# Kernel optimization log

Measured on AMD Instinct MI355X. Metric: run time of the kernel, lower is better.

Reference implementation:

```python
import jax, jax.numpy as jnp
import numpy as np

B, F, NQ, DT, TS, K = 16384, 256, 2048, 256, 16, 8
GH, SH, CALH = 128, 128, 16
SPD = DT + TS
SPH = max(int(SPD * 0.25), 16)
CD = DT + 3 + TS + 3  # h_base + y_base + 3 gate stats + z_top + |d_safe| + |d_spec| = 278
CH = max(int(CD * 0.25), 16)
RES_SCALE = 0.1


def _ln(x, g, b):
    m = x.mean(-1, keepdims=True)
    v = ((x - m) ** 2).mean(-1, keepdims=True)
    return (x - m) * jax.lax.rsqrt(v + 1e-5) * g + b


def _resmlp(x, lg, lb, w1, b1, w2, b2):
    h = jnp.maximum(_ln(x, lg, lb) @ w1 + b1, 0.0)
    return h @ w2 + b2


def setup_inputs() -> dict:
    key = jax.random.key(0)
    ks = iter(jax.random.split(key, 48))
    def nrm(shape, s=0.05):
        return jax.random.normal(next(ks), shape, jnp.float32) * s
    d = {}
    d["x_num"] = jax.random.normal(next(ks), (B, F), jnp.float32)
    d["robust_center"] = nrm((1, F), 0.1)
    d["robust_scale"] = jax.random.uniform(next(ks), (1, F), jnp.float32, 0.5, 1.5)
    d["quantile_sorted"] = jnp.sort(jax.random.normal(next(ks), (NQ, F), jnp.float32), axis=0)
    d["stem_w1"] = nrm((3, CALH)); d["stem_b1"] = jnp.zeros((CALH,))
    d["stem_w2"] = nrm((CALH, CALH)); d["stem_b2"] = jnp.zeros((CALH,))
    d["stem_w3"] = nrm((CALH, 1)); d["stem_b3"] = jnp.zeros((1,))
    d["gate_w1"] = nrm((F, GH)); d["gate_b1"] = jnp.zeros((GH,))
    d["gate_w2"] = nrm((GH, F)); d["gate_b2"] = jnp.zeros((F,))
    d["bb_w"] = nrm((F, DT)); d["bb_b"] = jnp.zeros((DT,))
    d["base_w"] = nrm((DT, 1)); d["base_b"] = jnp.zeros((1,))
    d["safe_lg"] = jnp.ones((DT,)); d["safe_lb"] = jnp.zeros((DT,))
    d["safe_w1"] = nrm((DT, SH)); d["safe_b1"] = jnp.zeros((SH,))
    d["safe_w2"] = nrm((SH, 1)); d["safe_b2"] = jnp.zeros((1,))
    d["top_w1"] = nrm((1, TS)); d["top_b1"] = jnp.zeros((TS,))
    d["top_w2"] = nrm((TS, TS)); d["top_b2"] = jnp.zeros((TS,))
    d["spec_lg"] = jnp.ones((SPD,)); d["spec_lb"] = jnp.zeros((SPD,))
    d["spec_w1"] = nrm((SPD, SPH)); d["spec_b1"] = jnp.zeros((SPH,))
    d["spec_w2"] = nrm((SPH, 1)); d["spec_b2"] = jnp.zeros((1,))
    d["conf_lg"] = jnp.ones((CD,)); d["conf_lb"] = jnp.zeros((CD,))
    d["conf_w1"] = nrm((CD, CH)); d["conf_b1"] = jnp.zeros((CH,))
    d["conf_w2"] = nrm((CH, 1)); d["conf_b2"] = jnp.full((1,), -2.0)  # gamma_init_bias
    return d


def _forward(x_num, robust_center, robust_scale, quantile_sorted,
             stem_w1, stem_b1, stem_w2, stem_b2, stem_w3, stem_b3,
             gate_w1, gate_b1, gate_w2, gate_b2,
             bb_w, bb_b, base_w, base_b,
             safe_lg, safe_lb, safe_w1, safe_b1, safe_w2, safe_b2,
             top_w1, top_b1, top_w2, top_b2,
             spec_lg, spec_lb, spec_w1, spec_b1, spec_w2, spec_b2,
             conf_lg, conf_lb, conf_w1, conf_b1, conf_w2, conf_b2):
    # --- calibration views ---
    x_robust = (x_num - robust_center) / robust_scale
    ranks = jax.vmap(jnp.searchsorted, in_axes=(1, 1), out_axes=1)(
        jax.lax.stop_gradient(quantile_sorted), jax.lax.stop_gradient(x_num))  # [B,F] int
    x_quant = jnp.clip(ranks.astype(jnp.float32) / (NQ - 1.0), 0.0, 1.0)
    x_views = jnp.stack([x_num, x_robust, x_quant], axis=-1)  # [B,F,3]
    h = jnp.maximum(x_views @ stem_w1 + stem_b1, 0.0)
    h = jnp.maximum(h @ stem_w2 + stem_b2, 0.0)
    resid = jnp.tanh((h @ stem_w3 + stem_b3)[..., 0])
    x_cal = x_num + RES_SCALE * resid
    # --- input gate ---
    g = jax.nn.sigmoid(jnp.maximum(x_cal @ gate_w1 + gate_b1, 0.0) @ gate_w2 + gate_b2)
    x_gated = x_cal * g
    # --- backbone (stand-in for TMLPBackbone.encode_hidden) ---
    h_base = jnp.maximum(x_gated @ bb_w + bb_b, 0.0)  # [B,DT]
    y_base = h_base @ base_w + base_b  # [B,1]
    gate_mean = g.mean(axis=1, keepdims=True)
    gate_max = g.max(axis=1, keepdims=True)
    gate_std = g.std(axis=1, keepdims=True)  # ddof=0, matches unbiased=False
    delta_safe = _resmlp(h_base, safe_lg, safe_lb, safe_w1, safe_b1, safe_w2, safe_b2)
    # --- top-k feature gather ---
    topk_g, topk_idx = jax.lax.top_k(g, K)
    topk_x = jnp.take_along_axis(x_cal, topk_idx, axis=1)
    topk_w = topk_g / (topk_g.sum(axis=1, keepdims=True) + 1e-6)
    xw = (topk_x * topk_w)[..., None]  # [B,K,1]
    tok = jnp.maximum(xw @ top_w1 + top_b1, 0.0) @ top_w2 + top_b2  # [B,K,TS]
    z_top = tok.mean(axis=1)  # [B,TS]
    delta_spec = _resmlp(jnp.concatenate([h_base, z_top], axis=1),
                         spec_lg, spec_lb, spec_w1, spec_b1, spec_w2, spec_b2)
    conf_in = jnp.concatenate([h_base, y_base, gate_mean, gate_max, gate_std,
                               z_top, jnp.abs(delta_safe), jnp.abs(delta_spec)], axis=1)
    gamma = jax.nn.sigmoid(_resmlp(conf_in, conf_lg, conf_lb, conf_w1, conf_b1, conf_w2, conf_b2))
    return (y_base + delta_safe + gamma * delta_spec)[:, 0]


def reference(x_num, robust_center, robust_scale, quantile_sorted,
              stem_w1, stem_b1, stem_w2, stem_b2, stem_w3, stem_b3,
              gate_w1, gate_b1, gate_w2, gate_b2,
              bb_w, bb_b, base_w, base_b,
              safe_lg, safe_lb, safe_w1, safe_b1, safe_w2, safe_b2,
              top_w1, top_b1, top_w2, top_b2,
              spec_lg, spec_lb, spec_w1, spec_b1, spec_w2, spec_b2,
              conf_lg, conf_lb, conf_w1, conf_b1, conf_w2, conf_b2):
    return _forward(x_num, robust_center, robust_scale, quantile_sorted,
                    stem_w1, stem_b1, stem_w2, stem_b2, stem_w3, stem_b3,
                    gate_w1, gate_b1, gate_w2, gate_b2,
                    bb_w, bb_b, base_w, base_b,
                    safe_lg, safe_lb, safe_w1, safe_b1, safe_w2, safe_b2,
                    top_w1, top_b1, top_w2, top_b2,
                    spec_lg, spec_lb, spec_w1, spec_b1, spec_w2, spec_b2,
                    conf_lg, conf_lb, conf_w1, conf_b1, conf_w2, conf_b2)
```

## Files before the change

kernel.cpp:

```cpp
#include <hip/hip_runtime.h>
#include <math.h>

static constexpr int B  = 16384;
static constexpr int F  = 256;
static constexpr int NQ = 2048;
static constexpr int TS = 16;
static constexpr int KTOP = 8;
static constexpr int SPD = 272;
static constexpr int SPH = 68;
static constexpr int CD  = 278;
static constexpr int CH  = 69;

typedef __attribute__((ext_vector_type(8))) short bf16x8;
typedef __attribute__((ext_vector_type(4))) float f32x4;

__device__ inline short f2bf(float f) {
    unsigned u = __builtin_bit_cast(unsigned, f);
    unsigned r = (u + 0x7FFF + ((u >> 16) & 1)) >> 16;
    return (short)r;
}

__device__ inline float fast_tanh(float o) {
    o = fminf(fmaxf(o, -15.0f), 15.0f);
    float e = __expf(2.0f * o);
    return (e - 1.0f) / (e + 1.0f);
}

__device__ inline void prep_one(const float* W, short* T, int local,
                                int K, int N, int KP) {
    const int n = local / KP, k = local - n * KP;
    T[local] = (k < K && n < N) ? f2bf(W[k * N + n]) : (short)0;
}

__global__ __launch_bounds__(256) void k_prepall(
    const float* __restrict__ gate_w1, const float* __restrict__ gate_w2,
    const float* __restrict__ bb_w,    const float* __restrict__ safe_w1,
    const float* __restrict__ spec_w1, const float* __restrict__ conf_w1,
    const float* __restrict__ qs,
    short* __restrict__ w1t, short* __restrict__ w2t, short* __restrict__ bbt,
    short* __restrict__ sw1t, short* __restrict__ spw1t, short* __restrict__ cfw1t,
    float* __restrict__ qs_t)
{
    const int idx = blockIdx.x * 256 + threadIdx.x;
    if (idx < 32768)       prep_one(gate_w1, w1t,  idx,           256, 128, 256);
    else if (idx < 65536)  prep_one(gate_w2, w2t,  idx - 32768,   128, 256, 128);
    else if (idx < 131072) prep_one(bb_w,    bbt,  idx - 65536,   256, 256, 256);
    else if (idx < 163840) prep_one(safe_w1, sw1t, idx - 131072,  256, 128, 256);
    else if (idx < 200704) prep_one(spec_w1, spw1t, idx - 163840, 272, 68, 288);
    else if (idx < 237568) prep_one(conf_w1, cfw1t, idx - 200704, 278, 69, 288);
    else if (idx < 761856) {
        const int local = idx - 237568;
        const int f = local >> 11, q = local & 2047;
        qs_t[local] = qs[q * 256 + f];
    }
}

__global__ __launch_bounds__(256) void k_calib5(
    const float* __restrict__ x_num, const float* __restrict__ center,
    const float* __restrict__ scale, const float* __restrict__ qs,
    const float* __restrict__ qs_t,
    const float* __restrict__ sw1, const float* __restrict__ sb1,
    const float* __restrict__ sw2, const float* __restrict__ sb2,
    const float* __restrict__ sw3, const float* __restrict__ sb3,
    float* __restrict__ x_cal)
{
    __shared__ float cq[63 * 256];
    const int tid = threadIdx.x;
    const int f = tid;
#pragma unroll 1
    for (int j = 0; j < 63; ++j)
        cq[j * 256 + tid] = qs[(32 * (j + 1)) * 256 + tid];
    __syncthreads();

    const float c = center[f];
    const float inv_sc = 1.0f / scale[f];
    const float* colp = qs_t + (long)f * NQ;
    const long row_base = (long)blockIdx.x * 32;

#pragma unroll 1
    for (int grp = 0; grp < 4; ++grp) {
        const long r0 = row_base + grp * 8;
        float x[8], xr[8];
#pragma unroll
        for (int i = 0; i < 8; ++i) {
            x[i] = x_num[(r0 + i) * F + f];
            xr[i] = (x[i] - c) * inv_sc;
        }
        int lo[8], hi[8];
#pragma unroll
        for (int i = 0; i < 8; ++i) { lo[i] = 0; hi[i] = 63; }
#pragma unroll
        for (int it = 0; it < 6; ++it) {
            float qv[8]; int mid[8];
#pragma unroll
            for (int i = 0; i < 8; ++i) {
                mid[i] = (lo[i] + hi[i]) >> 1;
                qv[i] = cq[mid[i] * 256 + f];
            }
#pragma unroll
            for (int i = 0; i < 8; ++i) {
                if (qv[i] < x[i]) lo[i] = mid[i] + 1; else hi[i] = mid[i];
            }
        }
        int base[8];
        {
            float pm[8];
#pragma unroll
            for (int i = 0; i < 8; ++i) pm[i] = colp[lo[i] * 32 + 16];
#pragma unroll
            for (int i = 0; i < 8; ++i)
                base[i] = lo[i] * 32 + ((pm[i] < x[i]) ? 16 : 0);
        }
        float xq[8];
#pragma unroll
        for (int i = 0; i < 8; ++i) {
            const float4* wp = reinterpret_cast<const float4*>(&colp[base[i]]);
            const float4 a = wp[0], b = wp[1], d = wp[2], e = wp[3];
            int cN = 0;
            cN += (a.x < x[i]); cN += (a.y < x[i]); cN += (a.z < x[i]); cN += (a.w < x[i]);
            cN += (b.x < x[i]); cN += (b.y < x[i]); cN += (b.z < x[i]); cN += (b.w < x[i]);
            cN += (d.x < x[i]); cN += (d.y < x[i]); cN += (d.z < x[i]); cN += (d.w < x[i]);
            cN += (e.x < x[i]); cN += (e.y < x[i]); cN += (e.z < x[i]); cN += (e.w < x[i]);
            const int rank = base[i] + cN;
            xq[i] = fminf((float)rank * (1.0f / (float)(NQ - 1)), 1.0f);
        }
#pragma unroll
        for (int hgrp = 0; hgrp < 2; ++hgrp) {
            const int o4 = hgrp * 4;
            float h2[4][16];
#pragma unroll
            for (int j = 0; j < 16; ++j) {
                const float bb = sb2[j];
#pragma unroll
                for (int i = 0; i < 4; ++i) h2[i][j] = bb;
            }
#pragma unroll 4
            for (int i16 = 0; i16 < 16; ++i16) {
                const float w0 = sw1[i16], w1v = sw1[16 + i16], w2v = sw1[32 + i16];
                const float bb = sb1[i16];
                float h1v[4];
#pragma unroll
                for (int i = 0; i < 4; ++i)
                    h1v[i] = fmaxf(bb + x[o4 + i] * w0 + xr[o4 + i] * w1v + xq[o4 + i] * w2v, 0.0f);
                float wv[16];
                const float4* wr = reinterpret_cast<const float4*>(&sw2[i16 * 16]);
                *reinterpret_cast<float4*>(&wv[0])  = wr[0];
                *reinterpret_cast<float4*>(&wv[4])  = wr[1];
                *reinterpret_cast<float4*>(&wv[8])  = wr[2];
                *reinterpret_cast<float4*>(&wv[12]) = wr[3];
#pragma unroll
                for (int j = 0; j < 16; ++j) {
#pragma unroll
                    for (int i = 0; i < 4; ++i) h2[i][j] += h1v[i] * wv[j];
                }
            }
            const float b3 = sb3[0];
            float o[4] = {b3, b3, b3, b3};
#pragma unroll
            for (int j = 0; j < 16; ++j) {
                const float w3v = sw3[j];
#pragma unroll
                for (int i = 0; i < 4; ++i) o[i] += fmaxf(h2[i][j], 0.0f) * w3v;
            }
#pragma unroll
            for (int i = 0; i < 4; ++i)
                x_cal[(r0 + o4 + i) * F + f] = x[o4 + i] + 0.1f * fast_tanh(o[i]);
        }
    }
}

static constexpr int ST1 = 136;
static constexpr int ST2 = 264;

__global__ __launch_bounds__(256) void k_fused(
    const float* __restrict__ x_cal,
    const short* __restrict__ w1t, const float* __restrict__ gate_b1,
    const short* __restrict__ w2t, const float* __restrict__ gate_b2,
    const short* __restrict__ bbt, const float* __restrict__ bb_b,
    float* __restrict__ g, float* __restrict__ h_b)
{
    __shared__ short s_c1[32 * ST1];
    __shared__ short s_xg[32 * ST2];

    const int tid = threadIdx.x;
    const int wave = tid >> 6, lane = tid & 63;
    const int sub = lane & 15, quad = lane >> 4;
    const int wm = wave & 1, wn = wave >> 1;
    const long row0 = (long)blockIdx.x * 32;
    const long mrow = row0 + wm * 16 + sub;

    {
        f32x4 acc[4];
#pragma unroll
        for (int t = 0; t < 4; ++t) acc[t] = (f32x4){0, 0, 0, 0};
#pragma unroll
        for (int k0 = 0; k0 < 256; k0 += 32) {
            const float* ap = x_cal + mrow * 256 + k0 + quad * 8;
            float av[8];
            *reinterpret_cast<float4*>(&av[0]) = *reinterpret_cast<const float4*>(ap);
            *reinterpret_cast<float4*>(&av[4]) = *reinterpret_cast<const float4*>(ap + 4);
            bf16x8 af;
#pragma unroll
            for (int j = 0; j < 8; ++j) af[j] = f2bf(av[j]);
#pragma unroll
            for (int t = 0; t < 4; ++t) {
                const int col = wn * 64 + t * 16 + sub;
                const bf16x8 bf = *reinterpret_cast<const bf16x8*>(
                    &w1t[(long)col * 256 + k0 + quad * 8]);
                acc[t] = __builtin_amdgcn_mfma_f32_16x16x32_bf16(af, bf, acc[t], 0, 0, 0);
            }
        }
#pragma unroll
        for (int t = 0; t < 4; ++t) {
            const int col = wn * 64 + t * 16 + sub;
            const float bb = gate_b1[col];
#pragma unroll
            for (int r = 0; r < 4; ++r) {
                const int rowl = wm * 16 + quad * 4 + r;
                s_c1[rowl * ST1 + col] = f2bf(fmaxf(acc[t][r] + bb, 0.0f));
            }
        }
    }
    __syncthreads();

    {
        f32x4 acc[8];
#pragma unroll
        for (int t = 0; t < 8; ++t) acc[t] = (f32x4){0, 0, 0, 0};
#pragma unroll
        for (int k0 = 0; k0 < 128; k0 += 32) {
            const bf16x8 af = *reinterpret_cast<const bf16x8*>(
                &s_c1[(wm * 16 + sub) * ST1 + k0 + quad * 8]);
#pragma unroll
            for (int t = 0; t < 8; ++t) {
                const int col = wn * 128 + t * 16 + sub;
                const bf16x8 bf = *reinterpret_cast<const bf16x8*>(
                    &w2t[(long)col * 128 + k0 + quad * 8]);
                acc[t] = __builtin_amdgcn_mfma_f32_16x16x32_bf16(af, bf, acc[t], 0, 0, 0);
            }
        }
#pragma unroll
        for (int t = 0; t < 8; ++t) {
            const int col = wn * 128 + t * 16 + sub;
            const float bb = gate_b2[col];
#pragma unroll
            for (int r = 0; r < 4; ++r) {
                const int rowl = wm * 16 + quad * 4 + r;
                const float gv = 1.0f / (1.0f + __expf(-(acc[t][r] + bb)));
                g[(row0 + rowl) * 256 + col] = gv;
                const float xg = x_cal[(row0 + rowl) * 256 + col] * gv;
                s_xg[rowl * ST2 + col] = f2bf(xg);
            }
        }
    }
    __syncthreads();

    {
        f32x4 acc[8];
#pragma unroll
        for (int t = 0; t < 8; ++t) acc[t] = (f32x4){0, 0, 0, 0};
#pragma unroll
        for (int k0 = 0; k0 < 256; k0 += 32) {
            const bf16x8 af = *reinterpret_cast<const bf16x8*>(
                &s_xg[(wm * 16 + sub) * ST2 + k0 + quad * 8]);
#pragma unroll
            for (int t = 0; t < 8; ++t) {
                const int col = wn * 128 + t * 16 + sub;
                const bf16x8 bf = *reinterpret_cast<const bf16x8*>(
                    &bbt[(long)col * 256 + k0 + quad * 8]);
                acc[t] = __builtin_amdgcn_mfma_f32_16x16x32_bf16(af, bf, acc[t], 0, 0, 0);
            }
        }
#pragma unroll
        for (int t = 0; t < 8; ++t) {
            const int col = wn * 128 + t * 16 + sub;
            const float bb = bb_b[col];
#pragma unroll
            for (int r = 0; r < 4; ++r) {
                const int rowl = wm * 16 + quad * 4 + r;
                h_b[(row0 + rowl) * 256 + col] = fmaxf(acc[t][r] + bb, 0.0f);
            }
        }
    }
}

__global__ __launch_bounds__(64) void k_topk(
    const float* __restrict__ g, const float* __restrict__ x_cal,
    const float* __restrict__ tw1, const float* __restrict__ tb1,
    const float* __restrict__ tw2, const float* __restrict__ tb2,
    float* __restrict__ z_top, float* __restrict__ stats)
{
    __shared__ float s_hm[16];
    const int b = blockIdx.x;
    const int lane = threadIdx.x;
    const long base = (long)b * F;

    float gv[4];
#pragma unroll
    for (int i = 0; i < 4; ++i) gv[i] = g[base + lane + 64 * i];

    float s = gv[0] + gv[1] + gv[2] + gv[3];
    float mx = fmaxf(fmaxf(gv[0], gv[1]), fmaxf(gv[2], gv[3]));
    for (int m = 32; m; m >>= 1) {
        s  += __shfl_xor(s, m);
        mx  = fmaxf(mx, __shfl_xor(mx, m));
    }
    const float mean = s * (1.0f / 256.0f);
    float vs = 0.0f;
#pragma unroll
    for (int i = 0; i < 4; ++i) { float d = gv[i] - mean; vs += d * d; }
    for (int m = 32; m; m >>= 1) vs += __shfl_xor(vs, m);
    const float stdv = sqrtf(vs * (1.0f / 256.0f));

    float cur[4]; int curi[4];
#pragma unroll
    for (int i = 0; i < 4; ++i) { cur[i] = gv[i]; curi[i] = lane + 64 * i; }
    float tv[KTOP]; int ti[KTOP]; float vsum = 0.0f;
    for (int r = 0; r < KTOP; ++r) {
        float bv = cur[0]; int bi = curi[0];
#pragma unroll
        for (int i = 1; i < 4; ++i)
            if (cur[i] > bv || (cur[i] == bv && curi[i] < bi)) { bv = cur[i]; bi = curi[i]; }
        for (int m = 32; m; m >>= 1) {
            float ov = __shfl_xor(bv, m);
            int   oi = __shfl_xor(bi, m);
            if (ov > bv || (ov == bv && oi < bi)) { bv = ov; bi = oi; }
        }
        tv[r] = bv; ti[r] = bi; vsum += bv;
#pragma unroll
        for (int i = 0; i < 4; ++i) if (curi[i] == bi) cur[i] = -INFINITY;
    }
    const float denom = 1.0f / (vsum + 1e-6f);

    if (lane < 16) {
        float hm = 0.0f;
        for (int k = 0; k < KTOP; ++k) {
            const float xk = x_cal[base + ti[k]];
            const float xw = xk * (tv[k] * denom);
            hm += fmaxf(xw * tw1[lane] + tb1[lane], 0.0f);
        }
        s_hm[lane] = hm * (1.0f / (float)KTOP);
    }
    __syncthreads();
    if (lane < 16) {
        float z = tb2[lane];
#pragma unroll
        for (int j = 0; j < 16; ++j) z += s_hm[j] * tw2[j * 16 + lane];
        z_top[(long)b * TS + lane] = z;
    }
    if (lane == 0) {
        stats[(long)b * 4 + 0] = mean;
        stats[(long)b * 4 + 1] = mx;
        stats[(long)b * 4 + 2] = stdv;
    }
}

static constexpr int HST = 260;
static constexpr int AST = 312;

template<int KP>
__device__ __forceinline__ void head_mfma16(
    const short* sa, const short* __restrict__ Wt,
    const float* __restrict__ b1v, const float* __restrict__ w2v, int Nreal,
    float (*s_red)[16], int wave, int sub, int quad)
{
    f32x4 acc[2];
#pragma unroll
    for (int t = 0; t < 2; ++t) acc[t] = (f32x4){0, 0, 0, 0};
#pragma unroll
    for (int k0 = 0; k0 < KP; k0 += 32) {
        const bf16x8 af = *reinterpret_cast<const bf16x8*>(
            &sa[sub * AST + k0 + quad * 8]);
#pragma unroll
        for (int t = 0; t < 2; ++t) {
            const int col = wave * 32 + t * 16 + sub;
            const bf16x8 bf = *reinterpret_cast<const bf16x8*>(
                &Wt[(long)col * KP + k0 + quad * 8]);
            acc[t] = __builtin_amdgcn_mfma_f32_16x16x32_bf16(af, bf, acc[t], 0, 0, 0);
        }
    }
    float rsum[4] = {0, 0, 0, 0};
#pragma unroll
    for (int t = 0; t < 2; ++t) {
        const int col = wave * 32 + t * 16 + sub;
        const float bb = (col < Nreal) ? b1v[col] : 0.0f;
        const float ww = (col < Nreal) ? w2v[col] : 0.0f;
#pragma unroll
        for (int rr = 0; rr < 4; ++rr)
            rsum[rr] += fmaxf(acc[t][rr] + bb, 0.0f) * ww;
    }
#pragma unroll
    for (int rr = 0; rr < 4; ++rr)
        for (int m = 1; m < 16; m <<= 1) rsum[rr] += __shfl_xor(rsum[rr], m);
    if (sub == 0) {
#pragma unroll
        for (int rr = 0; rr < 4; ++rr)
            s_red[wave][quad * 4 + rr] = rsum[rr];
    }
}

__global__ __launch_bounds__(256) void k_tail3(
    const float* __restrict__ h_base, const float* __restrict__ z_top,
    const float* __restrict__ gstats,
    const float* __restrict__ base_w, const float* __restrict__ base_b,
    const float* __restrict__ safe_lg, const float* __restrict__ safe_lb,
    const short* __restrict__ sw1t, const float* __restrict__ safe_b1,
    const float* __restrict__ safe_w2, const float* __restrict__ safe_b2,
    const float* __restrict__ spec_lg, const float* __restrict__ spec_lb,
    const short* __restrict__ spw1t, const float* __restrict__ spec_b1,
    const float* __restrict__ spec_w2, const float* __restrict__ spec_b2,
    const float* __restrict__ conf_lg, const float* __restrict__ conf_lb,
    const short* __restrict__ cfw1t, const float* __restrict__ conf_b1,
    const float* __restrict__ conf_w2, const float* __restrict__ conf_b2,
    float* __restrict__ out)
{
    __shared__ float s_h[16 * HST];
    __shared__ short s_a[16 * AST];
    __shared__ float s_z[16 * 16];
    __shared__ float s_g[16 * 4];
    __shared__ float s_sc[16 * 14];
    __shared__ float s_red[4][16];

    const int tid = threadIdx.x;
    const int wave = tid >> 6, lane = tid & 63;
    const int sub = lane & 15, quad = lane >> 4;
    const long row0 = (long)blockIdx.x * 16;

    for (int idx = tid; idx < 16 * 64; idx += 256) {
        const int r = idx >> 6, q = idx & 63;
        *reinterpret_cast<float4*>(&s_h[r * HST + q * 4]) =
            *reinterpret_cast<const float4*>(&h_base[(row0 + r) * 256 + q * 4]);
    }
    if (tid < 256) s_z[tid] = z_top[row0 * 16 + tid];
    if (tid < 64) s_g[tid] = gstats[row0 * 4 + tid];
    __syncthreads();

    {
        const int r = tid >> 4, l16 = tid & 15;
        float S = 0.0f, SS = 0.0f, Y = 0.0f;
#pragma unroll
        for (int i = 0; i < 16; ++i) {
            const int k = l16 + 16 * i;
            const float v = s_h[r * HST + k];
            S += v; SS += v * v; Y += v * base_w[k];
        }
        const float z0 = s_z[r * 16 + l16];
        float Sz = z0, SSz = z0 * z0;
#pragma unroll
        for (int m = 1; m < 16; m <<= 1) {
            S += __shfl_xor(S, m); SS += __shfl_xor(SS, m); Y += __shfl_xor(Y, m);
            Sz += __shfl_xor(Sz, m); SSz += __shfl_xor(SSz, m);
        }
        if (l16 == 0) {
            float* sc = &s_sc[r * 14];
            sc[0] = S; sc[1] = SS; sc[2] = Sz; sc[3] = SSz;
            sc[4] = Y + base_b[0];
            const float mu = S * (1.0f / 256.0f);
            sc[5] = mu;
            sc[6] = rsqrtf(SS * (1.0f / 256.0f) - mu * mu + 1e-5f);
            const float musp = (S + Sz) * (1.0f / (float)SPD);
            sc[7] = musp;
            sc[8] = rsqrtf((SS + SSz) * (1.0f / (float)SPD) - musp * musp + 1e-5f);
        }
    }
    __syncthreads();

    for (int idx = tid; idx < 16 * 128; idx += 256) {
        const int r = idx >> 7, k = (idx & 127) * 2;
        const float mu = s_sc[r * 14 + 5], rs = s_sc[r * 14 + 6];
        const float v0 = (s_h[r * HST + k] - mu) * rs * safe_lg[k] + safe_lb[k];
        const float v1 = (s_h[r * HST + k + 1] - mu) * rs * safe_lg[k + 1] + safe_lb[k + 1];
        const unsigned pk = (unsigned)(unsigned short)f2bf(v0) |
                            ((unsigned)(unsigned short)f2bf(v1) << 16);
        *reinterpret_cast<unsigned*>(&s_a[r * AST + k]) = pk;
    }
    __syncthreads();

    head_mfma16<256>(s_a, sw1t, safe_b1, safe_w2, 128, s_red, wave, sub, quad);
    __syncthreads();

    if (tid < 16)
        s_sc[tid * 14 + 9] = s_red[0][tid] + s_red[1][tid] + s_red[2][tid] + s_red[3][tid] + safe_b2[0];
    for (int idx = tid; idx < 16 * 144; idx += 256) {
        const int r = idx / 144, k = (idx - r * 144) * 2;
        const float mu = s_sc[r * 14 + 7], rs = s_sc[r * 14 + 8];
        float vv[2];
#pragma unroll
        for (int h = 0; h < 2; ++h) {
            const int kk = k + h;
            float raw = (kk < 256) ? s_h[r * HST + kk]
                       : (kk < SPD) ? s_z[r * 16 + kk - 256] : 0.0f;
            vv[h] = (kk < SPD) ? (raw - mu) * rs * spec_lg[kk] + spec_lb[kk] : 0.0f;
        }
        const unsigned pk = (unsigned)(unsigned short)f2bf(vv[0]) |
                            ((unsigned)(unsigned short)f2bf(vv[1]) << 16);
        *reinterpret_cast<unsigned*>(&s_a[r * AST + k]) = pk;
    }
    __syncthreads();

    head_mfma16<288>(s_a, spw1t, spec_b1, spec_w2, SPH, s_red, wave, sub, quad);
    __syncthreads();

    if (tid < 16) {
        float* sc = &s_sc[tid * 14];
        const float dsp = s_red[0][tid] + s_red[1][tid] + s_red[2][tid] + s_red[3][tid] + spec_b2[0];
        sc[10] = dsp;
        const float yb = sc[4];
        const float gm = s_g[tid * 4 + 0], gx = s_g[tid * 4 + 1], gs = s_g[tid * 4 + 2];
        const float ads = fabsf(sc[9]), adp = fabsf(dsp);
        const float es = yb + gm + gx + gs + ads + adp;
        const float eq = yb * yb + gm * gm + gx * gx + gs * gs + ads * ads + adp * adp;
        const float muc = (sc[0] + sc[2] + es) * (1.0f / (float)CD);
        sc[11] = muc;
        sc[12] = rsqrtf((sc[1] + sc[3] + eq) * (1.0f / (float)CD) - muc * muc + 1e-5f);
    }
    __syncthreads();

    for (int idx = tid; idx < 16 * 144; idx += 256) {
        const int r = idx / 144, k = (idx - r * 144) * 2;
        const float mu = s_sc[r * 14 + 11], rs = s_sc[r * 14 + 12];
        float vv[2];
#pragma unroll
        for (int h = 0; h < 2; ++h) {
            const int kk = k + h;
            float raw;
            if (kk < 256)       raw = s_h[r * HST + kk];
            else if (kk == 256) raw = s_sc[r * 14 + 4];
            else if (kk == 257) raw = s_g[r * 4 + 0];
            else if (kk == 258) raw = s_g[r * 4 + 1];
            else if (kk == 259) raw = s_g[r * 4 + 2];
            else if (kk < 276)  raw = s_z[r * 16 + kk - 260];
            else if (kk == 276) raw = fabsf(s_sc[r * 14 + 9]);
            else if (kk == 277) raw = fabsf(s_sc[r * 14 + 10]);
            else                raw = 0.0f;
            vv[h] = (kk < CD) ? (raw - mu) * rs * conf_lg[kk] + conf_lb[kk] : 0.0f;
        }
        const unsigned pk = (unsigned)(unsigned short)f2bf(vv[0]) |
                            ((unsigned)(unsigned short)f2bf(vv[1]) << 16);
        *reinterpret_cast<unsigned*>(&s_a[r * AST + k]) = pk;
    }
    __syncthreads();

    head_mfma16<288>(s_a, cfw1t, conf_b1, conf_w2, CH, s_red, wave, sub, quad);
    __syncthreads();

    if (tid < 16) {
        const float* sc = &s_sc[tid * 14];
        const float gamma = 1.0f / (1.0f + __expf(
            -(s_red[0][tid] + s_red[1][tid] + s_red[2][tid] + s_red[3][tid] + conf_b2[0])));
        out[row0 + tid] = sc[4] + sc[9] + gamma * sc[10];
    }
}

extern "C" void kernel_launch(void* const* d_in, const int* in_sizes, int n_in,
                              void* d_out, int out_size, void* d_ws, size_t ws_size,
                              hipStream_t stream)
{
    const float* x_num   = (const float*)d_in[0];
    const float* center  = (const float*)d_in[1];
    const float* scale   = (const float*)d_in[2];
    const float* qs      = (const float*)d_in[3];
    const float* stem_w1 = (const float*)d_in[4];
    const float* stem_b1 = (const float*)d_in[5];
    const float* stem_w2 = (const float*)d_in[6];
    const float* stem_b2 = (const float*)d_in[7];
    const float* stem_w3 = (const float*)d_in[8];
    const float* stem_b3 = (const float*)d_in[9];
    const float* gate_w1 = (const float*)d_in[10];
    const float* gate_b1 = (const float*)d_in[11];
    const float* gate_w2 = (const float*)d_in[12];
    const float* gate_b2 = (const float*)d_in[13];
    const float* bb_w    = (const float*)d_in[14];
    const float* bb_b    = (const float*)d_in[15];
    const float* base_w  = (const float*)d_in[16];
    const float* base_b  = (const float*)d_in[17];
    const float* safe_lg = (const float*)d_in[18];
    const float* safe_lb = (const float*)d_in[19];
    const float* safe_w1 = (const float*)d_in[20];
    const float* safe_b1 = (const float*)d_in[21];
    const float* safe_w2 = (const float*)d_in[22];
    const float* safe_b2 = (const float*)d_in[23];
    const float* top_w1  = (const float*)d_in[24];
    const float* top_b1  = (const float*)d_in[25];
    const float* top_w2  = (const float*)d_in[26];
    const float* top_b2  = (const float*)d_in[27];
    const float* spec_lg = (const float*)d_in[28];
    const float* spec_lb = (const float*)d_in[29];
    const float* spec_w1 = (const float*)d_in[30];
    const float* spec_b1 = (const float*)d_in[31];
    const float* spec_w2 = (const float*)d_in[32];
    const float* spec_b2 = (const float*)d_in[33];
    const float* conf_lg = (const float*)d_in[34];
    const float* conf_lb = (const float*)d_in[35];
    const float* conf_w1 = (const float*)d_in[36];
    const float* conf_b1 = (const float*)d_in[37];
    const float* conf_w2 = (const float*)d_in[38];
    const float* conf_b2 = (const float*)d_in[39];

    float* ws    = (float*)d_ws;
    float* x_cal = ws;
    float* g_h   = x_cal + (long)B * 256;
    float* g     = g_h   + (long)B * 128;
    float* h_b   = g     + (long)B * 256;
    float* z_top = h_b   + (long)B * 256;
    float* gstat = z_top + (long)B * 16;
    short* w1t   = (short*)(gstat + (long)B * 4);
    short* w2t   = w1t   + 128 * 256;
    short* bbt   = w2t   + 256 * 128;
    short* sw1t  = bbt   + 256 * 256;
    short* spw1t = sw1t  + 128 * 256;
    short* cfw1t = spw1t + 128 * 288;
    float* qs_t  = h_b;
    float* out   = (float*)d_out;

    k_prepall<<<2976, 256, 0, stream>>>(gate_w1, gate_w2, bb_w, safe_w1, spec_w1,
                                        conf_w1, qs,
                                        w1t, w2t, bbt, sw1t, spw1t, cfw1t, qs_t);
    k_calib5<<<512, 256, 0, stream>>>(x_num, center, scale, qs, qs_t,
                                      stem_w1, stem_b1, stem_w2, stem_b2, stem_w3, stem_b3,
                                      x_cal);
    k_fused<<<512, 256, 0, stream>>>(x_cal, w1t, gate_b1, w2t, gate_b2, bbt, bb_b,
                                     g, h_b);
    k_topk<<<B, 64, 0, stream>>>(g, x_cal, top_w1, top_b1, top_w2, top_b2, z_top, gstat);
    k_tail3<<<B / 16, 256, 0, stream>>>(h_b, z_top, gstat,
                                        base_w, base_b,
                                        safe_lg, safe_lb, sw1t, safe_b1, safe_w2, safe_b2,
                                        spec_lg, spec_lb, spw1t, spec_b1, spec_w2, spec_b2,
                                        conf_lg, conf_lb, cfw1t, conf_b1, conf_w2, conf_b2,
                                        out);
}
```

Measured before the change: 311.9 us.

## Pipeline calib quantile search, emit bf16 activations, pack topk rows per block

The calibration kernel now prefetches and coarse-searches the next row group while counting and running the stem MLP on the current group, so global quantile loads overlap compute. It also writes a bf16 copy of the calibrated input, which the gate/backbone kernel reads directly instead of loading fp32 and converting. The top-k kernel processes four rows per 256-thread block and replaces the shared-memory reduction and barrier with wave shuffles. This raises register pressure in calib and adds a slight extra rounding of x before gating.

```diff
diff --git a/kernel.cpp b/kernel.cpp
--- a/kernel.cpp
+++ b/kernel.cpp
@@ -18,6 +18,9 @@
     unsigned u = __builtin_bit_cast(unsigned, f);
     unsigned r = (u + 0x7FFF + ((u >> 16) & 1)) >> 16;
     return (short)r;
+}
+__device__ inline float bf2f(short s) {
+    return __builtin_bit_cast(float, ((unsigned)(unsigned short)s) << 16);
 }
 
 __device__ inline float fast_tanh(float o) {
@@ -55,14 +58,14 @@
     }
 }
 
-__global__ __launch_bounds__(256) void k_calib5(
+__global__ __launch_bounds__(256) void k_calib6(
     const float* __restrict__ x_num, const float* __restrict__ center,
     const float* __restrict__ scale, const float* __restrict__ qs,
     const float* __restrict__ qs_t,
     const float* __restrict__ sw1, const float* __restrict__ sb1,
     const float* __restrict__ sw2, const float* __restrict__ sb2,
     const float* __restrict__ sw3, const float* __restrict__ sb3,
-    float* __restrict__ x_cal)
+    float* __restrict__ x_cal, short* __restrict__ x_bf)
 {
     __shared__ float cq[63 * 256];
     const int tid = threadIdx.x;
@@ -77,95 +80,138 @@
     const float* colp = qs_t + (long)f * NQ;
     const long row_base = (long)blockIdx.x * 32;
 
-#pragma unroll 1
-    for (int grp = 0; grp < 4; ++grp) {
-        const long r0 = row_base + grp * 8;
-        float x[8], xr[8];
-#pragma unroll
-        for (int i = 0; i < 8; ++i) {
-            x[i] = x_num[(r0 + i) * F + f];
-            xr[i] = (x[i] - c) * inv_sc;
-        }
-        int lo[8], hi[8];
-#pragma unroll
-        for (int i = 0; i < 8; ++i) { lo[i] = 0; hi[i] = 63; }
+    float x[2][8], xr[2][8], pm[2][8];
+    int lo[2][8];
+
+    auto loadx = [&](int slot, int g) {
+        const long r0 = row_base + g * 8;
+#pragma unroll
+        for (int i = 0; i < 8; ++i)
+            x[slot][i] = x_num[(r0 + i) * F + f];
+    };
+    auto coarse = [&](int slot) {
+#pragma unroll
+        for (int i = 0; i < 8; ++i) xr[slot][i] = (x[slot][i] - c) * inv_sc;
+        int l[8], h[8];
+#pragma unroll
+        for (int i = 0; i < 8; ++i) { l[i] = 0; h[i] = 63; }
 #pragma unroll
         for (int it = 0; it < 6; ++it) {
             float qv[8]; int mid[8];
 #pragma unroll
             for (int i = 0; i < 8; ++i) {
-                mid[i] = (lo[i] + hi[i]) >> 1;
+                mid[i] = (l[i] + h[i]) >> 1;
                 qv[i] = cq[mid[i] * 256 + f];
             }
 #pragma unroll
             for (int i = 0; i < 8; ++i) {
-                if (qv[i] < x[i]) lo[i] = mid[i] + 1; else hi[i] = mid[i];
-            }
-        }
+                if (qv[i] < x[slot][i]) l[i] = mid[i] + 1; else h[i] = mid[i];
+            }
+        }
+#pragma unroll
+        for (int i = 0; i < 8; ++i) lo[slot][i] = l[i];
+    };
+    auto probes = [&](int slot) {
+#pragma unroll
+        for (int i = 0; i < 8; ++i)
+            pm[slot][i] = colp[lo[slot][i] * 32 + 16];
+    };
+    auto cnt16 = [](const float4* ld, float xv) {
+        int cN = 0;
+#pragma unroll
+        for (int q = 0; q < 4; ++q) {
+            cN += (ld[q].x < xv); cN += (ld[q].y < xv);
+            cN += (ld[q].z < xv); cN += (ld[q].w < xv);
+        }
+        return cN;
+    };
+    auto stem4 = [&](const float* xx, const float* xxr, const float* xxq, long r0o) {
+        float h2[4][16];
+#pragma unroll
+        for (int j = 0; j < 16; ++j) {
+            const float bb = sb2[j];
+#pragma unroll
+            for (int i = 0; i < 4; ++i) h2[i][j] = bb;
+        }
+#pragma unroll 4
+        for (int i16 = 0; i16 < 16; ++i16) {
+            const float w0 = sw1[i16], w1v = sw1[16 + i16], w2v = sw1[32 + i16];
+            const float bb = sb1[i16];
+            float h1v[4];
+#pragma unroll
+            for (int i = 0; i < 4; ++i)
+                h1v[i] = fmaxf(bb + xx[i] * w0 + xxr[i] * w1v + xxq[i] * w2v, 0.0f);
+            float wv[16];
+            const float4* wr = reinterpret_cast<const float4*>(&sw2[i16 * 16]);
+            *reinterpret_cast<float4*>(&wv[0])  = wr[0];
+            *reinterpret_cast<float4*>(&wv[4])  = wr[1];
+            *reinterpret_cast<float4*>(&wv[8])  = wr[2];
+            *reinterpret_cast<float4*>(&wv[12]) = wr[3];
+#pragma unroll
+            for (int j = 0; j < 16; ++j) {
+#pragma unroll
+                for (int i = 0; i < 4; ++i) h2[i][j] += h1v[i] * wv[j];
+            }
+        }
+        const float b3 = sb3[0];
+        float o[4] = {b3, b3, b3, b3};
+#pragma unroll
+        for (int j = 0; j < 16; ++j) {
+            const float w3v = sw3[j];
+#pragma unroll
+            for (int i = 0; i < 4; ++i) o[i] += fmaxf(h2[i][j], 0.0f) * w3v;
+        }
+#pragma unroll
+        for (int i = 0; i < 4; ++i) {
+            const float xc = xx[i] + 0.1f * fast_tanh(o[i]);
+            x_cal[(r0o + i) * F + f] = xc;
+            x_bf[(r0o + i) * F + f] = f2bf(xc);
+        }
+    };
+
+    loadx(0, 0); coarse(0); probes(0);
+
+#pragma unroll 1
+    for (int g = 0; g < 4; ++g) {
+        const int cs = g & 1, ns = cs ^ 1;
+        const long r0 = row_base + g * 8;
+
         int base[8];
-        {
-            float pm[8];
-#pragma unroll
-            for (int i = 0; i < 8; ++i) pm[i] = colp[lo[i] * 32 + 16];
-#pragma unroll
-            for (int i = 0; i < 8; ++i)
-                base[i] = lo[i] * 32 + ((pm[i] < x[i]) ? 16 : 0);
-        }
+#pragma unroll
+        for (int i = 0; i < 8; ++i)
+            base[i] = lo[cs][i] * 32 + ((pm[cs][i] < x[cs][i]) ? 16 : 0);
+
+        float4 ldA[4][4];
+#pragma unroll
+        for (int i = 0; i < 4; ++i) {
+            const float4* wp = reinterpret_cast<const float4*>(&colp[base[i]]);
+            ldA[i][0] = wp[0]; ldA[i][1] = wp[1]; ldA[i][2] = wp[2]; ldA[i][3] = wp[3];
+        }
+
+        if (g < 3) { loadx(ns, g + 1); coarse(ns); probes(ns); }
+
         float xq[8];
 #pragma unroll
-        for (int i = 0; i < 8; ++i) {
-            const float4* wp = reinterpret_cast<const float4*>(&colp[base[i]]);
-            const float4 a = wp[0], b = wp[1], d = wp[2], e = wp[3];
-            int cN = 0;
-            cN += (a.x < x[i]); cN += (a.y < x[i]); cN += (a.z < x[i]); cN += (a.w < x[i]);
-            cN += (b.x < x[i]); cN += (b.y < x[i]); cN += (b.z < x[i]); cN += (b.w < x[i]);
-            cN += (d.x < x[i]); cN += (d.y < x[i]); cN += (d.z < x[i]); cN += (d.w < x[i]);
-            cN += (e.x < x[i]); cN += (e.y < x[i]); cN += (e.z < x[i]); cN += (e.w < x[i]);
-            const int rank = base[i] + cN;
+        for (int i = 0; i < 4; ++i) {
+            const int rank = base[i] + cnt16(ldA[i], x[cs][i]);
             xq[i] = fminf((float)rank * (1.0f / (float)(NQ - 1)), 1.0f);
         }
-#pragma unroll
-        for (int hgrp = 0; hgrp < 2; ++hgrp) {
-            const int o4 = hgrp * 4;
-            float h2[4][16];
-#pragma unroll
-            for (int j = 0; j < 16; ++j) {
-                const float bb = sb2[j];
-#pragma unroll
-                for (int i = 0; i < 4; ++i) h2[i][j] = bb;
-            }
-#pragma unroll 4
-            for (int i16 = 0; i16 < 16; ++i16) {
-                const float w0 = sw1[i16], w1v = sw1[16 + i16], w2v = sw1[32 + i16];
-                const float bb = sb1[i16];
-                float h1v[4];
-#pragma unroll
-                for (int i = 0; i < 4; ++i)
-                    h1v[i] = fmaxf(bb + x[o4 + i] * w0 + xr[o4 + i] * w1v + xq[o4 + i] * w2v, 0.0f);
-                float wv[16];
-                const float4* wr = reinterpret_cast<const float4*>(&sw2[i16 * 16]);
-                *reinterpret_cast<float4*>(&wv[0])  = wr[0];
-                *reinterpret_cast<float4*>(&wv[4])  = wr[1];
-                *reinterpret_cast<float4*>(&wv[8])  = wr[2];
-                *reinterpret_cast<float4*>(&wv[12]) = wr[3];
-#pragma unroll
-                for (int j = 0; j < 16; ++j) {
-#pragma unroll
-                    for (int i = 0; i < 4; ++i) h2[i][j] += h1v[i] * wv[j];
-                }
-            }
-            const float b3 = sb3[0];
-            float o[4] = {b3, b3, b3, b3};
-#pragma unroll
-            for (int j = 0; j < 16; ++j) {
-                const float w3v = sw3[j];
-#pragma unroll
-                for (int i = 0; i < 4; ++i) o[i] += fmaxf(h2[i][j], 0.0f) * w3v;
-            }
-#pragma unroll
-            for (int i = 0; i < 4; ++i)
-                x_cal[(r0 + o4 + i) * F + f] = x[o4 + i] + 0.1f * fast_tanh(o[i]);
-        }
+
+        float4 ldB[4][4];
+#pragma unroll
+        for (int i = 0; i < 4; ++i) {
+            const float4* wp = reinterpret_cast<const float4*>(&colp[base[4 + i]]);
+            ldB[i][0] = wp[0]; ldB[i][1] = wp[1]; ldB[i][2] = wp[2]; ldB[i][3] = wp[3];
+        }
+
+        stem4(&x[cs][0], &xr[cs][0], &xq[0], r0);
+
+#pragma unroll
+        for (int i = 0; i < 4; ++i) {
+            const int rank = base[4 + i] + cnt16(ldB[i], x[cs][4 + i]);
+            xq[4 + i] = fminf((float)rank * (1.0f / (float)(NQ - 1)), 1.0f);
+        }
+        stem4(&x[cs][4], &xr[cs][4], &xq[4], r0 + 4);
     }
 }
 
@@ -173,7 +219,7 @@
 static constexpr int ST2 = 264;
 
 __global__ __launch_bounds__(256) void k_fused(
-    const float* __restrict__ x_cal,
+    const short* __restrict__ x_bf,
     const short* __restrict__ w1t, const float* __restrict__ gate_b1,
     const short* __restrict__ w2t, const float* __restrict__ gate_b2,
     const short* __restrict__ bbt, const float* __restrict__ bb_b,
@@ -195,13 +241,8 @@
         for (int t = 0; t < 4; ++t) acc[t] = (f32x4){0, 0, 0, 0};
 #pragma unroll
         for (int k0 = 0; k0 < 256; k0 += 32) {
-            const float* ap = x_cal + mrow * 256 + k0 + quad * 8;
-            float av[8];
-            *reinterpret_cast<float4*>(&av[0]) = *reinterpret_cast<const float4*>(ap);
-            *reinterpret_cast<float4*>(&av[4]) = *reinterpret_cast<const float4*>(ap + 4);
-            bf16x8 af;
-#pragma unroll
-            for (int j = 0; j < 8; ++j) af[j] = f2bf(av[j]);
+            const bf16x8 af = *reinterpret_cast<const bf16x8*>(
+                &x_bf[mrow * 256 + k0 + quad * 8]);
 #pragma unroll
             for (int t = 0; t < 4; ++t) {
                 const int col = wn * 64 + t * 16 + sub;
@@ -248,8 +289,8 @@
                 const int rowl = wm * 16 + quad * 4 + r;
                 const float gv = 1.0f / (1.0f + __expf(-(acc[t][r] + bb)));
                 g[(row0 + rowl) * 256 + col] = gv;
-                const float xg = x_cal[(row0 + rowl) * 256 + col] * gv;
-                s_xg[rowl * ST2 + col] = f2bf(xg);
+                const float xv = bf2f(x_bf[(row0 + rowl) * 256 + col]);
+                s_xg[rowl * ST2 + col] = f2bf(xv * gv);
             }
         }
     }
@@ -284,16 +325,15 @@
     }
 }
 
-__global__ __launch_bounds__(64) void k_topk(
+__global__ __launch_bounds__(256) void k_topk2(
     const float* __restrict__ g, const float* __restrict__ x_cal,
     const float* __restrict__ tw1, const float* __restrict__ tb1,
     const float* __restrict__ tw2, const float* __restrict__ tb2,
     float* __restrict__ z_top, float* __restrict__ stats)
 {
-    __shared__ float s_hm[16];
-    const int b = blockIdx.x;
-    const int lane = threadIdx.x;
-    const long base = (long)b * F;
+    const int wave = threadIdx.x >> 6, lane = threadIdx.x & 63;
+    const long b = (long)blockIdx.x * 4 + wave;
+    const long base = b * F;
 
     float gv[4];
 #pragma unroll
@@ -332,26 +372,26 @@
     }
     const float denom = 1.0f / (vsum + 1e-6f);
 
+    float hm = 0.0f;
     if (lane < 16) {
-        float hm = 0.0f;
         for (int k = 0; k < KTOP; ++k) {
             const float xk = x_cal[base + ti[k]];
             const float xw = xk * (tv[k] * denom);
             hm += fmaxf(xw * tw1[lane] + tb1[lane], 0.0f);
         }
-        s_hm[lane] = hm * (1.0f / (float)KTOP);
-    }
-    __syncthreads();
-    if (lane < 16) {
-        float z = tb2[lane];
-#pragma unroll
-        for (int j = 0; j < 16; ++j) z += s_hm[j] * tw2[j * 16 + lane];
-        z_top[(long)b * TS + lane] = z;
-    }
+        hm *= (1.0f / (float)KTOP);
+    }
+    float z = (lane < 16) ? tb2[lane] : 0.0f;
+#pragma unroll
+    for (int j = 0; j < 16; ++j) {
+        const float hj = __shfl(hm, j);
+        if (lane < 16) z += hj * tw2[j * 16 + lane];
+    }
+    if (lane < 16) z_top[b * TS + lane] = z;
     if (lane == 0) {
-        stats[(long)b * 4 + 0] = mean;
-        stats[(long)b * 4 + 1] = mx;
-        stats[(long)b * 4 + 2] = stdv;
+        stats[b * 4 + 0] = mean;
+        stats[b * 4 + 1] = mx;
+        stats[b * 4 + 2] = stdv;
     }
 }
 
@@ -611,17 +651,19 @@
     short* spw1t = sw1t  + 128 * 256;
     short* cfw1t = spw1t + 128 * 288;
     float* qs_t  = h_b;
+    short* x_bf  = (short*)g_h;
     float* out   = (float*)d_out;
 
     k_prepall<<<2976, 256, 0, stream>>>(gate_w1, gate_w2, bb_w, safe_w1, spec_w1,
                                         conf_w1, qs,
                                         w1t, w2t, bbt, sw1t, spw1t, cfw1t, qs_t);
-    k_calib5<<<512, 256, 0, stream>>>(x_num, center, scale, qs, qs_t,
+    k_calib6<<<512, 256, 0, stream>>>(x_num, center, scale, qs, qs_t,
                                       stem_w1, stem_b1, stem_w2, stem_b2, stem_w3, stem_b3,
-                                      x_cal);
-    k_fused<<<512, 256, 0, stream>>>(x_cal, w1t, gate_b1, w2t, gate_b2, bbt, bb_b,
+                                      x_cal, x_bf);
+    k_fused<<<512, 256, 0, stream>>>(x_bf, w1t, gate_b1, w2t, gate_b2, bbt, bb_b,
                                      g, h_b);
-    k_topk<<<B, 64, 0, stream>>>(g, x_cal, top_w1, top_b1, top_w2, top_b2, z_top, gstat);
+    k_topk2<<<B / 4, 256, 0, stream>>>(g, x_cal, top_w1, top_b1, top_w2, top_b2,
+                                       z_top, gstat);
     k_tail3<<<B / 16, 256, 0, stream>>>(h_b, z_top, gstat,
                                         base_w, base_b,
                                         safe_lg, safe_lb, sw1t, safe_b1, safe_w2, safe_b2,
```

New measurement: 317.4 us. No clear change (+1.7%).

## Store calibrated features as bf16, split calib rows across two half-blocks, batch topk waves

Applied to the files above, without the earlier changes.

The calibration kernel now writes x_cal as bf16 rather than fp32, which halves that write and the reads in the fused GEMM and top-k kernels and removes the per-element conversion inside the GEMM. The calibration kernel runs 512 threads per block, with each half handling 16 rows, so it has more waves in flight. Top-k now packs four rows per block, one per wave, and swaps the shared-memory sync for wave shuffles. In exchange, the gated x*g product and the top-k gather use bf16-rounded x, which adds a small precision loss there.

```diff
diff --git a/kernel.cpp b/kernel.cpp
--- a/kernel.cpp
+++ b/kernel.cpp
@@ -18,6 +18,9 @@
     unsigned u = __builtin_bit_cast(unsigned, f);
     unsigned r = (u + 0x7FFF + ((u >> 16) & 1)) >> 16;
     return (short)r;
+}
+__device__ inline float bf2f(short s) {
+    return __builtin_bit_cast(float, ((unsigned)(unsigned short)s) << 16);
 }
 
 __device__ inline float fast_tanh(float o) {
@@ -55,30 +58,31 @@
     }
 }
 
-__global__ __launch_bounds__(256) void k_calib5(
+__global__ __launch_bounds__(512, 4) void k_calib7(
     const float* __restrict__ x_num, const float* __restrict__ center,
     const float* __restrict__ scale, const float* __restrict__ qs,
     const float* __restrict__ qs_t,
     const float* __restrict__ sw1, const float* __restrict__ sb1,
     const float* __restrict__ sw2, const float* __restrict__ sb2,
     const float* __restrict__ sw3, const float* __restrict__ sb3,
-    float* __restrict__ x_cal)
+    short* __restrict__ x_bf)
 {
     __shared__ float cq[63 * 256];
     const int tid = threadIdx.x;
-    const int f = tid;
+    const int f = tid & 255;
+    const int half = tid >> 8;
 #pragma unroll 1
-    for (int j = 0; j < 63; ++j)
-        cq[j * 256 + tid] = qs[(32 * (j + 1)) * 256 + tid];
+    for (int j = half; j < 63; j += 2)
+        cq[j * 256 + f] = qs[(32 * (j + 1)) * 256 + f];
     __syncthreads();
 
     const float c = center[f];
     const float inv_sc = 1.0f / scale[f];
     const float* colp = qs_t + (long)f * NQ;
-    const long row_base = (long)blockIdx.x * 32;
+    const long row_base = (long)blockIdx.x * 32 + half * 16;
 
 #pragma unroll 1
-    for (int grp = 0; grp < 4; ++grp) {
+    for (int grp = 0; grp < 2; ++grp) {
         const long r0 = row_base + grp * 8;
         float x[8], xr[8];
 #pragma unroll
@@ -163,8 +167,10 @@
                 for (int i = 0; i < 4; ++i) o[i] += fmaxf(h2[i][j], 0.0f) * w3v;
             }
 #pragma unroll
-            for (int i = 0; i < 4; ++i)
-                x_cal[(r0 + o4 + i) * F + f] = x[o4 + i] + 0.1f * fast_tanh(o[i]);
+            for (int i = 0; i < 4; ++i) {
+                const float xc = x[o4 + i] + 0.1f * fast_tanh(o[i]);
+                x_bf[(r0 + o4 + i) * F + f] = f2bf(xc);
+            }
         }
     }
 }
@@ -173,7 +179,7 @@
 static constexpr int ST2 = 264;
 
 __global__ __launch_bounds__(256) void k_fused(
-    const float* __restrict__ x_cal,
+    const short* __restrict__ x_bf,
     const short* __restrict__ w1t, const float* __restrict__ gate_b1,
     const short* __restrict__ w2t, const float* __restrict__ gate_b2,
     const short* __restrict__ bbt, const float* __restrict__ bb_b,
@@ -195,13 +201,8 @@
         for (int t = 0; t < 4; ++t) acc[t] = (f32x4){0, 0, 0, 0};
 #pragma unroll
         for (int k0 = 0; k0 < 256; k0 += 32) {
-            const float* ap = x_cal + mrow * 256 + k0 + quad * 8;
-            float av[8];
-            *reinterpret_cast<float4*>(&av[0]) = *reinterpret_cast<const float4*>(ap);
-            *reinterpret_cast<float4*>(&av[4]) = *reinterpret_cast<const float4*>(ap + 4);
-            bf16x8 af;
-#pragma unroll
-            for (int j = 0; j < 8; ++j) af[j] = f2bf(av[j]);
+            const bf16x8 af = *reinterpret_cast<const bf16x8*>(
+                &x_bf[mrow * 256 + k0 + quad * 8]);
 #pragma unroll
             for (int t = 0; t < 4; ++t) {
                 const int col = wn * 64 + t * 16 + sub;
@@ -248,8 +249,8 @@
                 const int rowl = wm * 16 + quad * 4 + r;
                 const float gv = 1.0f / (1.0f + __expf(-(acc[t][r] + bb)));
                 g[(row0 + rowl) * 256 + col] = gv;
-                const float xg = x_cal[(row0 + rowl) * 256 + col] * gv;
-                s_xg[rowl * ST2 + col] = f2bf(xg);
+                const float xv = bf2f(x_bf[(row0 + rowl) * 256 + col]);
+                s_xg[rowl * ST2 + col] = f2bf(xv * gv);
             }
         }
     }
@@ -284,16 +285,15 @@
     }
 }
 
-__global__ __launch_bounds__(64) void k_topk(
-    const float* __restrict__ g, const float* __restrict__ x_cal,
+__global__ __launch_bounds__(256) void k_topk2(
+    const float* __restrict__ g, const short* __restrict__ x_bf,
     const float* __restrict__ tw1, const float* __restrict__ tb1,
     const float* __restrict__ tw2, const float* __restrict__ tb2,
     float* __restrict__ z_top, float* __restrict__ stats)
 {
-    __shared__ float s_hm[16];
-    const int b = blockIdx.x;
-    const int lane = threadIdx.x;
-    const long base = (long)b * F;
+    const int wave = threadIdx.x >> 6, lane = threadIdx.x & 63;
+    const long b = (long)blockIdx.x * 4 + wave;
+    const long base = b * F;
 
     float gv[4];
 #pragma unroll
@@ -332,26 +332,26 @@
     }
     const float denom = 1.0f / (vsum + 1e-6f);
 
+    float hm = 0.0f;
     if (lane < 16) {
-        float hm = 0.0f;
         for (int k = 0; k < KTOP; ++k) {
-            const float xk = x_cal[base + ti[k]];
+            const float xk = bf2f(x_bf[base + ti[k]]);
             const float xw = xk * (tv[k] * denom);
             hm += fmaxf(xw * tw1[lane] + tb1[lane], 0.0f);
         }
-        s_hm[lane] = hm * (1.0f / (float)KTOP);
-    }
-    __syncthreads();
-    if (lane < 16) {
-        float z = tb2[lane];
-#pragma unroll
-        for (int j = 0; j < 16; ++j) z += s_hm[j] * tw2[j * 16 + lane];
-        z_top[(long)b * TS + lane] = z;
-    }
+        hm *= (1.0f / (float)KTOP);
+    }
+    float z = (lane < 16) ? tb2[lane] : 0.0f;
+#pragma unroll
+    for (int j = 0; j < 16; ++j) {
+        const float hj = __shfl(hm, j);
+        if (lane < 16) z += hj * tw2[j * 16 + lane];
+    }
+    if (lane < 16) z_top[b * TS + lane] = z;
     if (lane == 0) {
-        stats[(long)b * 4 + 0] = mean;
-        stats[(long)b * 4 + 1] = mx;
-        stats[(long)b * 4 + 2] = stdv;
+        stats[b * 4 + 0] = mean;
+        stats[b * 4 + 1] = mx;
+        stats[b * 4 + 2] = stdv;
     }
 }
 
@@ -611,17 +611,19 @@
     short* spw1t = sw1t  + 128 * 256;
     short* cfw1t = spw1t + 128 * 288;
     float* qs_t  = h_b;
+    short* x_bf  = (short*)g_h;
     float* out   = (float*)d_out;
 
     k_prepall<<<2976, 256, 0, stream>>>(gate_w1, gate_w2, bb_w, safe_w1, spec_w1,
                                         conf_w1, qs,
                                         w1t, w2t, bbt, sw1t, spw1t, cfw1t, qs_t);
-    k_calib5<<<512, 256, 0, stream>>>(x_num, center, scale, qs, qs_t,
+    k_calib7<<<512, 512, 0, stream>>>(x_num, center, scale, qs, qs_t,
                                       stem_w1, stem_b1, stem_w2, stem_b2, stem_w3, stem_b3,
-                                      x_cal);
-    k_fused<<<512, 256, 0, stream>>>(x_cal, w1t, gate_b1, w2t, gate_b2, bbt, bb_b,
+                                      x_bf);
+    k_fused<<<512, 256, 0, stream>>>(x_bf, w1t, gate_b1, w2t, gate_b2, bbt, bb_b,
                                      g, h_b);
-    k_topk<<<B, 64, 0, stream>>>(g, x_cal, top_w1, top_b1, top_w2, top_b2, z_top, gstat);
+    k_topk2<<<B / 4, 256, 0, stream>>>(g, x_bf, top_w1, top_b1, top_w2, top_b2,
+                                       z_top, gstat);
     k_tail3<<<B / 16, 256, 0, stream>>>(h_b, z_top, gstat,
                                         base_w, base_b,
                                         safe_lg, safe_lb, sw1t, safe_b1, safe_w2, safe_b2,
```

Result: slower. 371.2 us (+19.0%).
